# Performance work log

Measured on AMD Instinct MI355X. Metric: run time of the kernel, lower is better.

The kernel has to match this reference:

```python
import jax, jax.numpy as jnp
import numpy as np

N_NODES = 100000
N_EDGES = 1600000
F_IN, HID, N_CLS = 64, 64, 40


def setup_inputs() -> dict:
    key = jax.random.key(0)
    ks = jax.random.split(key, 8)
    feats = jax.random.normal(ks[0], (N_NODES, F_IN), dtype=jnp.float32)
    src = jax.random.randint(ks[1], (N_EDGES,), 0, N_NODES, dtype=jnp.int32)
    dst = jax.random.randint(ks[2], (N_EDGES,), 0, N_NODES, dtype=jnp.int32)
    def lin(k, out_d, in_d):
        s = 1.0 / np.sqrt(in_d)
        return jax.random.uniform(k, (out_d, in_d), jnp.float32, -s, s)
    return {
        "features": feats,
        "src": src,
        "dst": dst,
        "W0": lin(ks[3], HID, F_IN), "b0": jnp.zeros((HID,), jnp.float32),
        "W1": lin(ks[4], HID, HID), "b1": jnp.zeros((HID,), jnp.float32),
        "W2": lin(ks[5], N_CLS, HID), "b2": jnp.zeros((N_CLS,), jnp.float32),
    }


def reference(features, src, dst, W0, b0, W1, b1, W2, b2):
    n = features.shape[0]
    # in-degrees (gcn aggregator normalizes by deg + 1, counting self-loop)
    deg = jax.ops.segment_sum(jnp.ones_like(dst, dtype=features.dtype), dst,
                              num_segments=n)  # [N]
    inv = 1.0 / (deg + 1.0)  # [N]

    def sage_gcn(h, W, b, act):
        # gather src features, sum into dst: message passing
        neigh = jax.ops.segment_sum(h[src], dst, num_segments=n)  # [N, d]
        h_neigh = (neigh + h) * inv[:, None]
        out = h_neigh @ W.T + b
        return jax.nn.relu(out) if act else out

    h = sage_gcn(features, W0, b0, True)
    h = sage_gcn(h, W1, b1, True)   # dropout = identity in eval mode
    h = sage_gcn(h, W2, b2, False)
    return h
```

## Files before the change

### kernel.cpp

```cpp
#include <hip/hip_runtime.h>
#include <hip/hip_bf16.h>


#define N_FEAT 64
#define CAP 64
#define CAPB 8
#define BSH 9
#define BSZ 512
#define OVF_CAP 4096
#define OVL 1024

__device__ __forceinline__ float rl(float v, int l) {
    return __int_as_float(__builtin_amdgcn_readlane(__float_as_int(v), l));
}

__device__ __forceinline__ void bin_body(const int* __restrict__ src,
                                         const int* __restrict__ dst,
                                         unsigned int* __restrict__ bins,
                                         int* __restrict__ ovf, int* __restrict__ ovf_cnt,
                                         int n_edges, int nbk, int bid) {
    __shared__ int lcnt[256];
    __shared__ unsigned int lrec0[256];
    const int tid = threadIdx.x;
    lcnt[tid] = 0;
    __syncthreads();

    const int e = bid * 256 + tid;
    const bool valid = e < n_edges;
    int s = 0, d = 0;
    if (valid) { s = src[e]; d = dst[e]; }
    const int b = d >> BSH;
    const unsigned int pack = ((unsigned int)(d & (BSZ - 1)) << 17) | (unsigned int)s;

    if (valid) {
        int slot = atomicAdd(&lcnt[b], 1);
        if (slot == 0) {
            lrec0[b] = pack;
        } else if (slot < CAPB) {
            __builtin_nontemporal_store(pack, &bins[((size_t)bid * nbk + b) * CAPB + slot]);
        } else {
            int p = atomicAdd(ovf_cnt, 1);
            if (p < OVF_CAP) { ovf[2 * p] = s; ovf[2 * p + 1] = d; }
        }
    }
    __syncthreads();
    if (tid < nbk) {
        int c = lcnt[tid];
        c = (c < CAPB) ? c : CAPB;
        const unsigned int v0 = (c == 0) ? 0u : (lrec0[tid] | ((unsigned int)c << 26));
        __builtin_nontemporal_store(v0, &bins[((size_t)bid * nbk + tid) * CAPB]);
    }
}

__device__ __forceinline__ void transform64_body(const float* __restrict__ h,
                                                 const float* __restrict__ W,
                                                 float* __restrict__ t, int n_nodes, int bid) {
    const int lane = threadIdx.x & 63;
    const int wave = (bid << 2) | (threadIdx.x >> 6);
    float4 wreg[16];
    const float4* W4 = (const float4*)(W + lane * N_FEAT);
#pragma unroll
    for (int k = 0; k < 16; ++k) wreg[k] = W4[k];
    const float* wf = (const float*)wreg;

    const int node0 = wave * 8;
    for (int k = 0; k < 8; ++k) {
        const int node = node0 + k;
        if (node >= n_nodes) return;
        const float hv = h[(size_t)node * N_FEAT + lane];
        float acc = 0.f;
#pragma unroll
        for (int f = 0; f < 64; ++f) acc = fmaf(rl(hv, f), wf[f], acc);
        t[(size_t)node * N_FEAT + lane] = acc;
    }
}

__global__ __launch_bounds__(256) void prep(const int* __restrict__ src,
                                            const int* __restrict__ dst,
                                            unsigned int* __restrict__ bins,
                                            int* __restrict__ ovf, int* __restrict__ ovf_cnt,
                                            int n_edges, int nbk,
                                            const float* __restrict__ feats,
                                            const float* __restrict__ W0,
                                            float* __restrict__ t0, int n_nodes, int PB) {
    const int b = (int)blockIdx.x;
    if (b < PB)
        bin_body(src, dst, bins, ovf, ovf_cnt, n_edges, nbk, b);
    else
        transform64_body(feats, W0, t0, n_nodes, b - PB);
}

__global__ __launch_bounds__(1024) void fill_scan(const unsigned int* __restrict__ bins,
                                                  const int* __restrict__ ovf,
                                                  const int* __restrict__ ovf_cnt,
                                                  int* __restrict__ deg,
                                                  int* __restrict__ ell,
                                                  float* __restrict__ xz,
                                                  int nblk, int nbk, int n_nodes) {
    __shared__ int lell[BSZ * 32];
    __shared__ int lcnt[BSZ];
    __shared__ unsigned int lovf[OVL];
    __shared__ int lovn;
    const int tid = threadIdx.x;
    const int b = (int)blockIdx.x;
    const int base_node = b << BSH;

    for (int i = tid; i < BSZ * 32; i += 1024) lell[i] = n_nodes;
    if (tid < BSZ) lcnt[tid] = 0;
    if (tid == 0) lovn = 0;
    if (b == 0 && tid < 64) xz[tid] = 0.f;
    __syncthreads();

    const uint4* b4 = (const uint4*)bins;
    for (int seg = tid; seg < nblk; seg += 1024) {
        const size_t ro = ((size_t)seg * nbk + b) * 2;
        const uint4 r0 = b4[ro];
        const int n = (int)(r0.x >> 26);
        if (n == 0) continue;
        unsigned int rec[8];
        rec[0] = r0.x & 0x03FFFFFFu; rec[1] = r0.y; rec[2] = r0.z; rec[3] = r0.w;
        if (n > 4) {
            const uint4 r1 = b4[ro + 1];
            rec[4] = r1.x; rec[5] = r1.y; rec[6] = r1.z; rec[7] = r1.w;
        }
#pragma unroll
        for (int r = 0; r < CAPB; ++r) {
            if (r < n) {
                const unsigned int v = rec[r];
                const int ld = (int)((v >> 17) & (BSZ - 1));
                const int sv = (int)(v & 0x1FFFFu);
                const int slot = atomicAdd(&lcnt[ld], 1);
                if (slot < 32) {
                    lell[(ld << 5) + slot] = sv;
                } else if (slot < CAP) {
                    int p = atomicAdd(&lovn, 1);
                    if (p < OVL)
                        lovf[p] = (unsigned)sv | ((unsigned)ld << 17) |
                                  ((unsigned)(slot - 32) << 26);
                }
            }
        }
    }
    {
        int oc = *ovf_cnt; oc = (oc < OVF_CAP) ? oc : OVF_CAP;
        for (int i = tid; i < oc; i += 1024) {
            const int d = ovf[2 * i + 1];
            if ((d >> BSH) == b) {
                const int sv = ovf[2 * i];
                const int ld = d - base_node;
                const int slot = atomicAdd(&lcnt[ld], 1);
                if (slot < 32) {
                    lell[(ld << 5) + slot] = sv;
                } else if (slot < CAP) {
                    int p = atomicAdd(&lovn, 1);
                    if (p < OVL)
                        lovf[p] = (unsigned)sv | ((unsigned)ld << 17) |
                                  ((unsigned)(slot - 32) << 26);
                }
            }
        }
    }
    __syncthreads();
    for (int t = tid; t < BSZ; t += 1024) {
        const int node = base_node + t;
        if (node < n_nodes && lcnt[t] > 32) {
            int* p1 = &ell[((size_t)(n_nodes + node)) << 5];
            for (int j = 0; j < 32; ++j) p1[j] = n_nodes;
        }
    }
    __syncthreads();
    {
        int nn = lovn; nn = (nn < OVL) ? nn : OVL;
        for (int i = tid; i < nn; i += 1024) {
            const unsigned int v = lovf[i];
            const int sv = (int)(v & 0x1FFFFu);
            const int ld = (int)((v >> 17) & (BSZ - 1));
            const int sl = (int)(v >> 26);
            ell[(((size_t)(n_nodes + base_node + ld)) << 5) + sl] = sv;
        }
    }
    const int4* l4 = (const int4*)lell;
    int4* e4 = (int4*)(ell + ((size_t)base_node << 5));
    for (int i = tid; i < BSZ * 8; i += 1024) {
        const int node = base_node + (i >> 3);
        if (node < n_nodes) e4[i] = l4[i];
    }
    for (int t = tid; t < BSZ; t += 1024) {
        const int node = base_node + t;
        if (node < n_nodes) deg[node] = lcnt[t];
    }
}

template <int OUTW, int NPW>
__global__ __launch_bounds__(256, 4) void agg_t_k(const float* __restrict__ t,
                                                  const float* __restrict__ bias,
                                                  const float* __restrict__ Wn,
                                                  const int* __restrict__ deg,
                                                  const int* __restrict__ ell,
                                                  float* __restrict__ tn,
                                                  int n_nodes) {
    __shared__ float4 sW[64 * 17];
    if (blockIdx.x == 0 && threadIdx.x < OUTW)
        tn[(size_t)n_nodes * OUTW + threadIdx.x] = 0.f;
    {
        const float4* Wg = (const float4*)Wn;
        for (int i = threadIdx.x; i < OUTW * 16; i += 256)
            sW[(i >> 4) * 17 + (i & 15)] = Wg[i];
    }
    __syncthreads();

    const int lane = threadIdx.x & 63;
    const int w = threadIdx.x >> 6;
    const int wave = (blockIdx.x << 2) | w;
    const int g = lane >> 4;
    const int q = lane & 15;
    const float4* t4 = (const float4*)t;
    const float4* tq = t4 + q;
    const int4* ell4 = (const int4*)ell;
    const float4 bq = ((const float4*)bias)[q];
    const int wrow = (OUTW == 64) ? lane : ((lane < OUTW) ? lane : 0);
    const float4* wrow4 = sW + wrow * 17;
    const bool has_out = (OUTW == 64) || (lane < OUTW);

    const int node0 = wave * NPW;
    if (node0 >= n_nodes) return;
    const int gi = g * 2;

#define GATH8(V, I)                         \
    do {                                    \
        V[0] = tq[(size_t)(I)[0].x * 16];   \
        V[1] = tq[(size_t)(I)[0].y * 16];   \
        V[2] = tq[(size_t)(I)[0].z * 16];   \
        V[3] = tq[(size_t)(I)[0].w * 16];   \
        V[4] = tq[(size_t)(I)[1].x * 16];   \
        V[5] = tq[(size_t)(I)[1].y * 16];   \
        V[6] = tq[(size_t)(I)[1].z * 16];   \
        V[7] = tq[(size_t)(I)[1].w * 16];   \
    } while (0)

#define EPILOGUE_GEMM(R)                                  \
    float o0 = 0.f, o1 = 0.f;                             \
    _Pragma("unroll")                                     \
    for (int c = 0; c < 16; c += 2) {                     \
        float4 w0 = wrow4[c];                             \
        float4 w1 = wrow4[c + 1];                         \
        o0 = fmaf(rl((R).x, c), w0.x, o0);                \
        o0 = fmaf(rl((R).y, c), w0.y, o0);                \
        o0 = fmaf(rl((R).z, c), w0.z, o0);                \
        o0 = fmaf(rl((R).w, c), w0.w, o0);                \
        o1 = fmaf(rl((R).x, c + 1), w1.x, o1);            \
        o1 = fmaf(rl((R).y, c + 1), w1.y, o1);            \
        o1 = fmaf(rl((R).z, c + 1), w1.z, o1);            \
        o1 = fmaf(rl((R).w, c + 1), w1.w, o1);            \
    }

    if (node0 + NPW <= n_nodes) {
        int dgv[NPW];
#pragma unroll
        for (int k = 0; k < NPW; ++k) dgv[k] = deg[node0 + k];

        int4 ix[2][2];
        float4 vb[2][8];
        float4 selfb[2];
        ix[0][0] = ell4[(size_t)node0 * 8 + gi];
        ix[0][1] = ell4[(size_t)node0 * 8 + gi + 1];
        if (NPW > 1) {
            ix[1][0] = ell4[(size_t)(node0 + 1) * 8 + gi];
            ix[1][1] = ell4[(size_t)(node0 + 1) * 8 + gi + 1];
        }
        selfb[0] = t4[(size_t)node0 * 16 + q];
        GATH8(vb[0], ix[0]);

#pragma unroll
        for (int k = 0; k < NPW; ++k) {
            if (k + 1 < NPW) {
                selfb[(k + 1) & 1] = t4[(size_t)(node0 + k + 1) * 16 + q];
                GATH8(vb[(k + 1) & 1], ix[(k + 1) & 1]);
            }
            if (k + 2 < NPW) {
                ix[k & 1][0] = ell4[(size_t)(node0 + k + 2) * 8 + gi];
                ix[k & 1][1] = ell4[(size_t)(node0 + k + 2) * 8 + gi + 1];
            }
            const int node = node0 + k;
            const int d = dgv[k];
            const float4* v = vb[k & 1];
            float4 acc;
            acc.x = ((v[0].x + v[1].x) + (v[2].x + v[3].x)) +
                    ((v[4].x + v[5].x) + (v[6].x + v[7].x));
            acc.y = ((v[0].y + v[1].y) + (v[2].y + v[3].y)) +
                    ((v[4].y + v[5].y) + (v[6].y + v[7].y));
            acc.z = ((v[0].z + v[1].z) + (v[2].z + v[3].z)) +
                    ((v[4].z + v[5].z) + (v[6].z + v[7].z));
            acc.w = ((v[0].w + v[1].w) + (v[2].w + v[3].w)) +
                    ((v[4].w + v[5].w) + (v[6].w + v[7].w));

            if (d > 32) {
                int4 j0 = ell4[((size_t)(n_nodes + node)) * 8 + gi];
                int4 j1 = ell4[((size_t)(n_nodes + node)) * 8 + gi + 1];
                {
                    float4 u0 = tq[(size_t)j0.x * 16];
                    float4 u1 = tq[(size_t)j0.y * 16];
                    float4 u2 = tq[(size_t)j0.z * 16];
                    float4 u3 = tq[(size_t)j0.w * 16];
                    acc.x += (u0.x + u1.x) + (u2.x + u3.x);
                    acc.y += (u0.y + u1.y) + (u2.y + u3.y);
                    acc.z += (u0.z + u1.z) + (u2.z + u3.z);
                    acc.w += (u0.w + u1.w) + (u2.w + u3.w);
                }
                {
                    float4 u0 = tq[(size_t)j1.x * 16];
                    float4 u1 = tq[(size_t)j1.y * 16];
                    float4 u2 = tq[(size_t)j1.z * 16];
                    float4 u3 = tq[(size_t)j1.w * 16];
                    acc.x += (u0.x + u1.x) + (u2.x + u3.x);
                    acc.y += (u0.y + u1.y) + (u2.y + u3.y);
                    acc.z += (u0.z + u1.z) + (u2.z + u3.z);
                    acc.w += (u0.w + u1.w) + (u2.w + u3.w);
                }
            }

            acc.x += __shfl_xor(acc.x, 16, 64); acc.y += __shfl_xor(acc.y, 16, 64);
            acc.z += __shfl_xor(acc.z, 16, 64); acc.w += __shfl_xor(acc.w, 16, 64);
            acc.x += __shfl_xor(acc.x, 32, 64); acc.y += __shfl_xor(acc.y, 32, 64);
            acc.z += __shfl_xor(acc.z, 32, 64); acc.w += __shfl_xor(acc.w, 32, 64);

            const float invv = 1.0f / (float)(d + 1);
            float4 r;
            r.x = fmaxf((acc.x + selfb[k & 1].x) * invv + bq.x, 0.f);
            r.y = fmaxf((acc.y + selfb[k & 1].y) * invv + bq.y, 0.f);
            r.z = fmaxf((acc.z + selfb[k & 1].z) * invv + bq.z, 0.f);
            r.w = fmaxf((acc.w + selfb[k & 1].w) * invv + bq.w, 0.f);

            EPILOGUE_GEMM(r);
            if (has_out) tn[(size_t)node * OUTW + lane] = o0 + o1;
        }
    } else {
        for (int k = 0; k < NPW; ++k) {
            const int node = node0 + k;
            if (node >= n_nodes) return;
            const int d = deg[node];
            float4 acc = make_float4(0.f, 0.f, 0.f, 0.f);
            const int np = (d > 32) ? 2 : 1;
            for (int p = 0; p < np; ++p) {
                int4 ii[2];
                ii[0] = ell4[((size_t)p * n_nodes + node) * 8 + gi];
                ii[1] = ell4[((size_t)p * n_nodes + node) * 8 + gi + 1];
                float4 vv[8];
                GATH8(vv, ii);
                acc.x += ((vv[0].x + vv[1].x) + (vv[2].x + vv[3].x)) +
                         ((vv[4].x + vv[5].x) + (vv[6].x + vv[7].x));
                acc.y += ((vv[0].y + vv[1].y) + (vv[2].y + vv[3].y)) +
                         ((vv[4].y + vv[5].y) + (vv[6].y + vv[7].y));
                acc.z += ((vv[0].z + vv[1].z) + (vv[2].z + vv[3].z)) +
                         ((vv[4].z + vv[5].z) + (vv[6].z + vv[7].z));
                acc.w += ((vv[0].w + vv[1].w) + (vv[2].w + vv[3].w)) +
                         ((vv[4].w + vv[5].w) + (vv[6].w + vv[7].w));
            }
            acc.x += __shfl_xor(acc.x, 16, 64); acc.y += __shfl_xor(acc.y, 16, 64);
            acc.z += __shfl_xor(acc.z, 16, 64); acc.w += __shfl_xor(acc.w, 16, 64);
            acc.x += __shfl_xor(acc.x, 32, 64); acc.y += __shfl_xor(acc.y, 32, 64);
            acc.z += __shfl_xor(acc.z, 32, 64); acc.w += __shfl_xor(acc.w, 32, 64);
            float4 self = t4[(size_t)node * 16 + q];
            const float invv = 1.0f / (float)(d + 1);
            float4 r;
            r.x = fmaxf((acc.x + self.x) * invv + bq.x, 0.f);
            r.y = fmaxf((acc.y + self.y) * invv + bq.y, 0.f);
            r.z = fmaxf((acc.z + self.z) * invv + bq.z, 0.f);
            r.w = fmaxf((acc.w + self.w) * invv + bq.w, 0.f);
            EPILOGUE_GEMM(r);
            if (has_out) tn[(size_t)node * OUTW + lane] = o0 + o1;
        }
    }
#undef GATH8
#undef EPILOGUE_GEMM
}

template <int NPW>
__global__ __launch_bounds__(256) void agg40_k(const float* __restrict__ t,
                                               const float* __restrict__ bias,
                                               const int* __restrict__ deg,
                                               const int* __restrict__ ell,
                                               float* __restrict__ out, int n_nodes) {
    const int lane = threadIdx.x & 63;
    const int wave = (blockIdx.x << 2) | (threadIdx.x >> 6);
    const int g = lane / 10;
    const int q = lane - g * 10;
    const bool act = lane < 60;
    const float actf = act ? 1.f : 0.f;
    const float4* t4 = (const float4*)t;
    const float4 bq = ((const float4*)bias)[q];
    const int node0 = wave * NPW;
    if (node0 >= n_nodes) return;

    int nmax = NPW;
    if (node0 + NPW > n_nodes) nmax = n_nodes - node0;

    int dg[NPW];
#pragma unroll
    for (int k = 0; k < NPW; ++k) dg[k] = deg[node0 + ((k < nmax) ? k : 0)];

    auto eaddr = [&](int nd, int e) -> size_t {
        return (((size_t)(e >> 5) * n_nodes + nd) << 5) + (e & 31);
    };

    float4 vb[2][4];
    auto issue = [&](int slot, int k) {
        const int node = node0 + k;
        int i0 = ell[eaddr(node, g + 0)];
        int i1 = ell[eaddr(node, g + 6)];
        int i2 = ell[eaddr(node, g + 12)];
        int i3 = ell[eaddr(node, g + 18)];
        vb[slot][0] = t4[(size_t)i0 * 10 + q];
        vb[slot][1] = t4[(size_t)i1 * 10 + q];
        vb[slot][2] = t4[(size_t)i2 * 10 + q];
        vb[slot][3] = t4[(size_t)i3 * 10 + q];
    };

    issue(0, 0);
#pragma unroll
    for (int k = 0; k < NPW; ++k) {
        if (k + 1 < NPW) issue((k + 1) & 1, k + 1);
        if (k >= nmax) break;
        const int node = node0 + k;
        const int d = dg[k];
        const float4* v = vb[k & 1];
        float4 acc;
        acc.x = (v[0].x + v[1].x) + (v[2].x + v[3].x);
        acc.y = (v[0].y + v[1].y) + (v[2].y + v[3].y);
        acc.z = (v[0].z + v[1].z) + (v[2].z + v[3].z);
        acc.w = (v[0].w + v[1].w) + (v[2].w + v[3].w);

        const int dcap = (d < CAP) ? d : CAP;
        for (int u = 1; u * 24 < dcap; ++u) {
            const int eb = u * 24 + g;
            const bool k0 = act && (eb + 0 < d) && (eb + 0 < CAP);
            const bool k1 = act && (eb + 6 < d) && (eb + 6 < CAP);
            const bool k2 = act && (eb + 12 < d) && (eb + 12 < CAP);
            const bool k3 = act && (eb + 18 < d) && (eb + 18 < CAP);
            int i0 = k0 ? ell[eaddr(node, eb + 0)] : n_nodes;
            int i1 = k1 ? ell[eaddr(node, eb + 6)] : n_nodes;
            int i2 = k2 ? ell[eaddr(node, eb + 12)] : n_nodes;
            int i3 = k3 ? ell[eaddr(node, eb + 18)] : n_nodes;
            float4 w0 = t4[(size_t)i0 * 10 + q];
            float4 w1 = t4[(size_t)i1 * 10 + q];
            float4 w2 = t4[(size_t)i2 * 10 + q];
            float4 w3 = t4[(size_t)i3 * 10 + q];
            acc.x += (w0.x + w1.x) + (w2.x + w3.x);
            acc.y += (w0.y + w1.y) + (w2.y + w3.y);
            acc.z += (w0.z + w1.z) + (w2.z + w3.z);
            acc.w += (w0.w + w1.w) + (w2.w + w3.w);
        }

        acc.x *= actf; acc.y *= actf; acc.z *= actf; acc.w *= actf;
        acc.x += __shfl(acc.x, lane + 30, 64); acc.y += __shfl(acc.y, lane + 30, 64);
        acc.z += __shfl(acc.z, lane + 30, 64); acc.w += __shfl(acc.w, lane + 30, 64);
        float4 s1, s2;
        s1.x = __shfl(acc.x, lane + 10, 64); s2.x = __shfl(acc.x, lane + 20, 64);
        s1.y = __shfl(acc.y, lane + 10, 64); s2.y = __shfl(acc.y, lane + 20, 64);
        s1.z = __shfl(acc.z, lane + 10, 64); s2.z = __shfl(acc.z, lane + 20, 64);
        s1.w = __shfl(acc.w, lane + 10, 64); s2.w = __shfl(acc.w, lane + 20, 64);
        acc.x += s1.x + s2.x; acc.y += s1.y + s2.y;
        acc.z += s1.z + s2.z; acc.w += s1.w + s2.w;

        const float4 self = t4[(size_t)node * 10 + q];
        const float invv = 1.0f / (float)(d + 1);
        float4 r;
        r.x = (acc.x + self.x) * invv + bq.x;
        r.y = (acc.y + self.y) * invv + bq.y;
        r.z = (acc.z + self.z) * invv + bq.z;
        r.w = (acc.w + self.w) * invv + bq.w;
        if (lane < 10) ((float4*)out)[(size_t)node * 10 + q] = r;
    }
}

extern "C" void kernel_launch(void* const* d_in, const int* in_sizes, int n_in,
                              void* d_out, int out_size, void* d_ws, size_t ws_size,
                              hipStream_t stream) {
    const float* feats = (const float*)d_in[0];
    const int*   src   = (const int*)d_in[1];
    const int*   dst   = (const int*)d_in[2];
    const float* W0    = (const float*)d_in[3];
    const float* b0    = (const float*)d_in[4];
    const float* W1    = (const float*)d_in[5];
    const float* b1    = (const float*)d_in[6];
    const float* W2    = (const float*)d_in[7];
    const float* b2    = (const float*)d_in[8];
    float*       out   = (float*)d_out;

    const int N = in_sizes[0] / N_FEAT;
    const int E = in_sizes[1];
    const int NBLK = (E + 255) / 256;
    const int NBK = (N + BSZ - 1) >> BSH;

    char* p = (char*)d_ws;
    const size_t xb = ((size_t)N * N_FEAT + 64) * sizeof(float);
    float* X = (float*)p; p += xb;
    float* Y = (float*)p; p += xb;
    unsigned int* bins = (unsigned int*)Y;
    const size_t binsb = (size_t)NBLK * NBK * CAPB * sizeof(unsigned int);
    if (binsb > xb) p += binsb - xb;
    int* deg = (int*)p;     p += (size_t)N * sizeof(int);
    int* ovf_cnt = (int*)p; p += 16;
    int* ovf = (int*)p;     p += (size_t)OVF_CAP * 2 * sizeof(int);
    int* ell = (int*)p;     p += (size_t)N * CAP * sizeof(int);

    hipMemsetAsync(ovf_cnt, 0, sizeof(int), stream);

    constexpr int NPW = 4;
    const int PB = NBLK;
    const int TB = ((N + 7) / 8 + 3) / 4;
    const int ab = ((N + NPW - 1) / NPW + 3) / 4;

    prep<<<PB + TB, 256, 0, stream>>>(src, dst, bins, ovf, ovf_cnt,
                                      E, NBK, feats, W0, X, N, PB);
    fill_scan<<<NBK, 1024, 0, stream>>>(bins, ovf, ovf_cnt, deg, ell,
                                        X + (size_t)N * N_FEAT, NBLK, NBK, N);
    agg_t_k<64, NPW><<<ab, 256, 0, stream>>>(X, b0, W1, deg, ell, Y, N);
    agg_t_k<40, NPW><<<ab, 256, 0, stream>>>(Y, b1, W2, deg, ell, X, N);
    agg40_k<NPW><<<ab, 256, 0, stream>>>(X, b2, deg, ell, out, N);
}
```

Measured before the change: 345.4 us.

## Stage edge bins in LDS and write coalesced; XOR-swizzle weight tile in LDS

The binning pass now builds each block's per-bucket records entirely in shared memory and writes the whole bin slab out with coalesced 16-byte nontemporal stores. Previously each edge was scattered to global memory with its own store. Separately, the aggregation kernel replaces the padded (stride 17) weight layout in LDS with an XOR-swizzled stride-16 layout, which reduces LDS size while still avoiding bank conflicts. The cost is more LDS in the bin kernel (8 KB per block) and an extra barrier, plus now writing unused bin slots to global memory.

New measurement: 330.6 us. 1.04x faster.

```diff
diff --git a/kernel.cpp b/kernel.cpp
--- a/kernel.cpp
+++ b/kernel.cpp
@@ -10,6 +10,8 @@
 #define OVF_CAP 4096
 #define OVL 1024
 
+typedef unsigned int u32x4 __attribute__((ext_vector_type(4)));
+
 __device__ __forceinline__ float rl(float v, int l) {
     return __int_as_float(__builtin_amdgcn_readlane(__float_as_int(v), l));
 }
@@ -20,7 +22,7 @@
                                          int* __restrict__ ovf, int* __restrict__ ovf_cnt,
                                          int n_edges, int nbk, int bid) {
     __shared__ int lcnt[256];
-    __shared__ unsigned int lrec0[256];
+    __shared__ unsigned int lbin[256 * CAPB];
     const int tid = threadIdx.x;
     lcnt[tid] = 0;
     __syncthreads();
@@ -34,10 +36,8 @@
 
     if (valid) {
         int slot = atomicAdd(&lcnt[b], 1);
-        if (slot == 0) {
-            lrec0[b] = pack;
-        } else if (slot < CAPB) {
-            __builtin_nontemporal_store(pack, &bins[((size_t)bid * nbk + b) * CAPB + slot]);
+        if (slot < CAPB) {
+            lbin[(b << 3) + slot] = pack;
         } else {
             int p = atomicAdd(ovf_cnt, 1);
             if (p < OVF_CAP) { ovf[2 * p] = s; ovf[2 * p + 1] = d; }
@@ -47,9 +47,14 @@
     if (tid < nbk) {
         int c = lcnt[tid];
         c = (c < CAPB) ? c : CAPB;
-        const unsigned int v0 = (c == 0) ? 0u : (lrec0[tid] | ((unsigned int)c << 26));
-        __builtin_nontemporal_store(v0, &bins[((size_t)bid * nbk + tid) * CAPB]);
-    }
+        const unsigned int v0 = lbin[tid << 3];
+        lbin[tid << 3] = c ? (v0 | ((unsigned int)c << 26)) : 0u;
+    }
+    __syncthreads();
+    u32x4* dst4 = (u32x4*)&bins[(size_t)bid * nbk * CAPB];
+    const u32x4* l4 = (const u32x4*)lbin;
+    for (int i = tid; i < nbk * 2; i += 256)
+        __builtin_nontemporal_store(l4[i], &dst4[i]);
 }
 
 __device__ __forceinline__ void transform64_body(const float* __restrict__ h,
@@ -199,13 +204,15 @@
                                                   const int* __restrict__ ell,
                                                   float* __restrict__ tn,
                                                   int n_nodes) {
-    __shared__ float4 sW[64 * 17];
+    __shared__ float4 sW[OUTW * 16];
     if (blockIdx.x == 0 && threadIdx.x < OUTW)
         tn[(size_t)n_nodes * OUTW + threadIdx.x] = 0.f;
     {
         const float4* Wg = (const float4*)Wn;
-        for (int i = threadIdx.x; i < OUTW * 16; i += 256)
-            sW[(i >> 4) * 17 + (i & 15)] = Wg[i];
+        for (int i = threadIdx.x; i < OUTW * 16; i += 256) {
+            const int row = i >> 4, col = i & 15;
+            sW[(row << 4) + (col ^ (row & 15))] = Wg[i];
+        }
     }
     __syncthreads();
 
@@ -219,7 +226,8 @@
     const int4* ell4 = (const int4*)ell;
     const float4 bq = ((const float4*)bias)[q];
     const int wrow = (OUTW == 64) ? lane : ((lane < OUTW) ? lane : 0);
-    const float4* wrow4 = sW + wrow * 17;
+    const float4* wrow4 = sW + (wrow << 4);
+    const int sx = wrow & 15;
     const bool has_out = (OUTW == 64) || (lane < OUTW);
 
     const int node0 = wave * NPW;
@@ -242,8 +250,8 @@
     float o0 = 0.f, o1 = 0.f;                             \
     _Pragma("unroll")                                     \
     for (int c = 0; c < 16; c += 2) {                     \
-        float4 w0 = wrow4[c];                             \
-        float4 w1 = wrow4[c + 1];                         \
+        float4 w0 = wrow4[c ^ sx];                        \
+        float4 w1 = wrow4[(c + 1) ^ sx];                  \
         o0 = fmaf(rl((R).x, c), w0.x, o0);                \
         o0 = fmaf(rl((R).y, c), w0.y, o0);                \
         o0 = fmaf(rl((R).z, c), w0.z, o0);                \
@@ -504,7 +512,7 @@
     int* ovf = (int*)p;     p += (size_t)OVF_CAP * 2 * sizeof(int);
     int* ell = (int*)p;     p += (size_t)N * CAP * sizeof(int);
 
-    hipMemsetAsync(ovf_cnt, 0, sizeof(int), stream);
+    (void)hipMemsetAsync(ovf_cnt, 0, sizeof(int), stream);
 
     constexpr int NPW = 4;
     const int PB = NBLK;
```
